# Kernel tuning notes

Hardware: AMD Instinct MI355X
Metric: run time of the kernel (lower is better)

Reference implementation:

```python
import jax, jax.numpy as jnp
import numpy as np

TEMPERATURE = 0.02


def setup_inputs() -> dict:
    key = jax.random.key(0)
    kq, kp = jax.random.split(key)
    query_embeddings = jax.random.normal(kq, (32, 32, 128), dtype=jnp.float32)      # [b, s, h]
    positive_embeddings = jax.random.normal(kp, (512, 128, 128), dtype=jnp.float32)  # [c, d, h]
    return {"query_embeddings": query_embeddings, "positive_embeddings": positive_embeddings}


def reference(query_embeddings, positive_embeddings):
    # Late interaction: all query tokens vs all doc tokens across the (in-)batch.
    # [b, c, s, d]
    late = jnp.einsum('bsh,cdh->bcsd', query_embeddings, positive_embeddings)
    # MaxSim: max over doc tokens, sum over query tokens -> [b, c]
    scores = late.max(axis=-1).sum(axis=-1) / TEMPERATURE
    # CrossEntropyLoss(reduction='mean') with labels = zeros(b)
    loss = jnp.mean(jax.nn.logsumexp(scores, axis=-1) - scores[:, 0])
    return loss
```

## Files before the change

kernel.cpp:

```cpp
#include <hip/hip_runtime.h>

#define BQ 32
#define H  128
#define C  512
#define D  128

typedef _Float16 half8v __attribute__((ext_vector_type(8)));
typedef float floatx4 __attribute__((ext_vector_type(4)));

__global__ __launch_bounds__(256) void qprep_kernel(const float* __restrict__ q,
                                                    _Float16* __restrict__ qs,
                                                    float* __restrict__ out) {
  int t = blockIdx.x * 256 + threadIdx.x;
  if (t == 0) out[0] = 0.0f;
  int lane = t & 63;
  int mt   = (t >> 6) & 1;
  int kb   = (t >> 7) & 3;
  int b    = t >> 9;
  int s    = mt * 16 + (lane & 15);
  int h    = kb * 32 + (lane >> 4) * 8;
  const float* src = q + ((b * 32 + s) * H + h);
  float4 v0 = *(const float4*)src;
  float4 v1 = *(const float4*)(src + 4);
  half8v o = { (_Float16)v0.x, (_Float16)v0.y, (_Float16)v0.z, (_Float16)v0.w,
               (_Float16)v1.x, (_Float16)v1.y, (_Float16)v1.z, (_Float16)v1.w };
  *(half8v*)(qs + (size_t)t * 8) = o;
}

__global__ __launch_bounds__(256, 2) void scores_kernel(const float* __restrict__ pos,
                                                        const _Float16* __restrict__ qs,
                                                        float* __restrict__ scores) {
  const int c    = blockIdx.x;
  const int tid  = threadIdx.x;
  const int w    = tid >> 6;
  const int lane = tid & 63;
  const int mt   = w & 1;
  const int half = w >> 1;
  const int ntg  = half * 4;
  const int quad = lane >> 4;
  const int nrow = lane & 15;

  __shared__ float pmm[BQ][2][32];

  const half8v* qf = (const half8v*)qs;
  const int abase  = mt * 64 + lane;
  const float* pc  = pos + (size_t)c * (D * H);

  half8v  bf[4][4];
  half8v  areg[2][4];
  floatx4 acc[2][4];

#pragma unroll
  for (int kb = 0; kb < 4; ++kb) areg[0][kb] = qf[abase + kb * 128];
#pragma unroll
  for (int kb = 0; kb < 4; ++kb) areg[1][kb] = qf[512 + abase + kb * 128];

#pragma unroll
  for (int kb = 0; kb < 4; ++kb)
#pragma unroll
    for (int nt = 0; nt < 4; ++nt) {
      const float* src = pc + ((ntg + nt) * 16 + nrow) * H + kb * 32 + quad * 8;
      float4 v0 = *(const float4*)src;
      float4 v1 = *(const float4*)(src + 4);
      half8v f = { (_Float16)v0.x, (_Float16)v0.y, (_Float16)v0.z, (_Float16)v0.w,
                   (_Float16)v1.x, (_Float16)v1.y, (_Float16)v1.z, (_Float16)v1.w };
      bf[kb][nt] = f;
    }

  auto reduce_store = [&](int b, floatx4* a) {
    float m0 = fmaxf(fmaxf(a[0][0], a[1][0]), fmaxf(a[2][0], a[3][0]));
    float m1 = fmaxf(fmaxf(a[0][1], a[1][1]), fmaxf(a[2][1], a[3][1]));
    float m2 = fmaxf(fmaxf(a[0][2], a[1][2]), fmaxf(a[2][2], a[3][2]));
    float m3 = fmaxf(fmaxf(a[0][3], a[1][3]), fmaxf(a[2][3], a[3][3]));
#pragma unroll
    for (int off = 1; off < 16; off <<= 1) {
      m0 = fmaxf(m0, __shfl_xor(m0, off));
      m1 = fmaxf(m1, __shfl_xor(m1, off));
      m2 = fmaxf(m2, __shfl_xor(m2, off));
      m3 = fmaxf(m3, __shfl_xor(m3, off));
    }
    if (nrow == 0) {
      float4 v = {m0, m1, m2, m3};
      *(float4*)&pmm[b][half][mt * 16 + quad * 4] = v;
    }
  };

#pragma unroll
  for (int nt = 0; nt < 4; ++nt) { floatx4 z = {0.f, 0.f, 0.f, 0.f}; acc[0][nt] = z; }
#pragma unroll
  for (int kb = 0; kb < 4; ++kb)
#pragma unroll
    for (int nt = 0; nt < 4; ++nt)
      acc[0][nt] = __builtin_amdgcn_mfma_f32_16x16x32_f16(areg[0][kb], bf[kb][nt], acc[0][nt], 0, 0, 0);

#pragma unroll
  for (int b = 1; b < BQ; ++b) {
    const int cur = b & 1, prv = cur ^ 1;
    if (b + 1 < BQ) {
      const int nb = (b + 1) * 512 + abase;
#pragma unroll
      for (int kb = 0; kb < 4; ++kb) areg[prv][kb] = qf[nb + kb * 128];
    }
#pragma unroll
    for (int nt = 0; nt < 4; ++nt) { floatx4 z = {0.f, 0.f, 0.f, 0.f}; acc[cur][nt] = z; }
#pragma unroll
    for (int kb = 0; kb < 4; ++kb)
#pragma unroll
      for (int nt = 0; nt < 4; ++nt)
        acc[cur][nt] = __builtin_amdgcn_mfma_f32_16x16x32_f16(areg[cur][kb], bf[kb][nt], acc[cur][nt], 0, 0, 0);
    reduce_store(b - 1, acc[prv]);
  }
  reduce_store(BQ - 1, acc[1]);

  __syncthreads();

  {
    int b  = tid >> 3;
    int sq = tid & 7;
    float4 x = *(float4*)&pmm[b][0][sq * 4];
    float4 y = *(float4*)&pmm[b][1][sq * 4];
    float v = fmaxf(x.x, y.x) + fmaxf(x.y, y.y) + fmaxf(x.z, y.z) + fmaxf(x.w, y.w);
    v += __shfl_xor(v, 1);
    v += __shfl_xor(v, 2);
    v += __shfl_xor(v, 4);
    if ((tid & 7) == 0) scores[b * C + c] = v * 50.0f;
  }
}

__global__ __launch_bounds__(256) void loss_kernel(const float* __restrict__ scores,
                                                   float* __restrict__ out) {
  __shared__ float red[8];
  const int b = blockIdx.x, tid = threadIdx.x, w = tid >> 6, lane = tid & 63;
  const float* row = scores + b * C;
  float x0 = row[tid], x1 = row[tid + 256];
  float mx = fmaxf(x0, x1);
#pragma unroll
  for (int off = 1; off < 64; off <<= 1) mx = fmaxf(mx, __shfl_xor(mx, off));
  if (lane == 0) red[w] = mx;
  __syncthreads();
  float bmax = fmaxf(fmaxf(red[0], red[1]), fmaxf(red[2], red[3]));
  float e = __expf(x0 - bmax) + __expf(x1 - bmax);
#pragma unroll
  for (int off = 1; off < 64; off <<= 1) e += __shfl_xor(e, off);
  if (lane == 0) red[4 + w] = e;
  __syncthreads();
  if (tid == 0) {
    float s = red[4] + red[5] + red[6] + red[7];
    atomicAdd(out, (bmax + __logf(s) - row[0]) * (1.0f / 32.0f));
  }
}

extern "C" void kernel_launch(void* const* d_in, const int* in_sizes, int n_in,
                              void* d_out, int out_size, void* d_ws, size_t ws_size,
                              hipStream_t stream) {
  const float* q = (const float*)d_in[0];
  const float* p = (const float*)d_in[1];
  float* scores  = (float*)d_ws;
  _Float16* qs   = (_Float16*)((char*)d_ws + 65536);

  qprep_kernel<<<64, 256, 0, stream>>>(q, qs, (float*)d_out);
  scores_kernel<<<C, 256, 0, stream>>>(p, qs, scores);
  loss_kernel<<<32, 256, 0, stream>>>(scores, (float*)d_out);
}
```

Measured before the change: 99.64 us.

## Swap MFMA operand roles so doc tokens are rows, cutting max-reduction shuffles

The doc tokens now go in the MFMA A operand (M dimension) and the query tokens in the B operand (N dimension). Each wave owns 32 doc rows and computes both 16-query tiles. The max over doc tokens can then be taken largely within each lane's accumulator registers, needing two cross-lane shuffles per value instead of four butterfly steps on four values. Each wave now loads all query fragments per batch, which doubles its query register loads and adds a four-way max across waves in shared memory.

```diff
diff --git a/kernel.cpp b/kernel.cpp
--- a/kernel.cpp
+++ b/kernel.cpp
@@ -14,10 +14,10 @@
   int t = blockIdx.x * 256 + threadIdx.x;
   if (t == 0) out[0] = 0.0f;
   int lane = t & 63;
-  int mt   = (t >> 6) & 1;
+  int st   = (t >> 6) & 1;
   int kb   = (t >> 7) & 3;
   int b    = t >> 9;
-  int s    = mt * 16 + (lane & 15);
+  int s    = st * 16 + (lane & 15);
   int h    = kb * 32 + (lane >> 4) * 8;
   const float* src = q + ((b * 32 + s) * H + h);
   float4 v0 = *(const float4*)src;
@@ -34,80 +34,86 @@
   const int tid  = threadIdx.x;
   const int w    = tid >> 6;
   const int lane = tid & 63;
-  const int mt   = w & 1;
-  const int half = w >> 1;
-  const int ntg  = half * 4;
   const int quad = lane >> 4;
-  const int nrow = lane & 15;
+  const int mrow = lane & 15;
 
-  __shared__ float pmm[BQ][2][32];
+  __shared__ float pmm[BQ][4][32];
 
   const half8v* qf = (const half8v*)qs;
-  const int abase  = mt * 64 + lane;
-  const float* pc  = pos + (size_t)c * (D * H);
+  const float*  pc = pos + (size_t)c * (D * H);
 
-  half8v  bf[4][4];
-  half8v  areg[2][4];
-  floatx4 acc[2][4];
+  half8v  pa[2][4];
+  half8v  qb[2][2][4];
+  floatx4 acc[2][2][2];
 
 #pragma unroll
-  for (int kb = 0; kb < 4; ++kb) areg[0][kb] = qf[abase + kb * 128];
+  for (int nt = 0; nt < 2; ++nt)
 #pragma unroll
-  for (int kb = 0; kb < 4; ++kb) areg[1][kb] = qf[512 + abase + kb * 128];
+    for (int kb = 0; kb < 4; ++kb) {
+      qb[0][nt][kb] = qf[(kb * 2 + nt) * 64 + lane];
+      qb[1][nt][kb] = qf[(( (1 * 4) + kb) * 2 + nt) * 64 + lane];
+    }
 
 #pragma unroll
   for (int kb = 0; kb < 4; ++kb)
 #pragma unroll
-    for (int nt = 0; nt < 4; ++nt) {
-      const float* src = pc + ((ntg + nt) * 16 + nrow) * H + kb * 32 + quad * 8;
+    for (int mt2 = 0; mt2 < 2; ++mt2) {
+      const float* src = pc + ((w * 32 + mt2 * 16 + mrow) * H + kb * 32 + quad * 8);
       float4 v0 = *(const float4*)src;
       float4 v1 = *(const float4*)(src + 4);
       half8v f = { (_Float16)v0.x, (_Float16)v0.y, (_Float16)v0.z, (_Float16)v0.w,
                    (_Float16)v1.x, (_Float16)v1.y, (_Float16)v1.z, (_Float16)v1.w };
-      bf[kb][nt] = f;
+      pa[mt2][kb] = f;
     }
 
-  auto reduce_store = [&](int b, floatx4* a) {
-    float m0 = fmaxf(fmaxf(a[0][0], a[1][0]), fmaxf(a[2][0], a[3][0]));
-    float m1 = fmaxf(fmaxf(a[0][1], a[1][1]), fmaxf(a[2][1], a[3][1]));
-    float m2 = fmaxf(fmaxf(a[0][2], a[1][2]), fmaxf(a[2][2], a[3][2]));
-    float m3 = fmaxf(fmaxf(a[0][3], a[1][3]), fmaxf(a[2][3], a[3][3]));
-#pragma unroll
-    for (int off = 1; off < 16; off <<= 1) {
-      m0 = fmaxf(m0, __shfl_xor(m0, off));
-      m1 = fmaxf(m1, __shfl_xor(m1, off));
-      m2 = fmaxf(m2, __shfl_xor(m2, off));
-      m3 = fmaxf(m3, __shfl_xor(m3, off));
-    }
-    if (nrow == 0) {
-      float4 v = {m0, m1, m2, m3};
-      *(float4*)&pmm[b][half][mt * 16 + quad * 4] = v;
-    }
+  auto reduce_store = [&](int b, floatx4 (&a)[2][2]) {
+    float t0 = fmaxf(fmaxf(fmaxf(a[0][0][0], a[0][0][1]), fmaxf(a[0][0][2], a[0][0][3])),
+                     fmaxf(fmaxf(a[1][0][0], a[1][0][1]), fmaxf(a[1][0][2], a[1][0][3])));
+    float t1 = fmaxf(fmaxf(fmaxf(a[0][1][0], a[0][1][1]), fmaxf(a[0][1][2], a[0][1][3])),
+                     fmaxf(fmaxf(a[1][1][0], a[1][1][1]), fmaxf(a[1][1][2], a[1][1][3])));
+    t0 = fmaxf(t0, __shfl_xor(t0, 16));
+    t0 = fmaxf(t0, __shfl_xor(t0, 32));
+    t1 = fmaxf(t1, __shfl_xor(t1, 16));
+    t1 = fmaxf(t1, __shfl_xor(t1, 32));
+    float v = (lane < 16) ? t0 : t1;
+    if (lane < 32) pmm[b][w][lane] = v;
   };
 
 #pragma unroll
-  for (int nt = 0; nt < 4; ++nt) { floatx4 z = {0.f, 0.f, 0.f, 0.f}; acc[0][nt] = z; }
+  for (int mt2 = 0; mt2 < 2; ++mt2)
+#pragma unroll
+    for (int nt = 0; nt < 2; ++nt) { floatx4 z = {0.f, 0.f, 0.f, 0.f}; acc[0][mt2][nt] = z; }
 #pragma unroll
   for (int kb = 0; kb < 4; ++kb)
 #pragma unroll
-    for (int nt = 0; nt < 4; ++nt)
-      acc[0][nt] = __builtin_amdgcn_mfma_f32_16x16x32_f16(areg[0][kb], bf[kb][nt], acc[0][nt], 0, 0, 0);
+    for (int mt2 = 0; mt2 < 2; ++mt2)
+#pragma unroll
+      for (int nt = 0; nt < 2; ++nt)
+        acc[0][mt2][nt] = __builtin_amdgcn_mfma_f32_16x16x32_f16(
+            pa[mt2][kb], qb[0][nt][kb], acc[0][mt2][nt], 0, 0, 0);
 
 #pragma unroll
   for (int b = 1; b < BQ; ++b) {
     const int cur = b & 1, prv = cur ^ 1;
     if (b + 1 < BQ) {
-      const int nb = (b + 1) * 512 + abase;
 #pragma unroll
-      for (int kb = 0; kb < 4; ++kb) areg[prv][kb] = qf[nb + kb * 128];
+      for (int nt = 0; nt < 2; ++nt)
+#pragma unroll
+        for (int kb = 0; kb < 4; ++kb)
+          qb[prv][nt][kb] = qf[(((b + 1) * 4 + kb) * 2 + nt) * 64 + lane];
     }
 #pragma unroll
-    for (int nt = 0; nt < 4; ++nt) { floatx4 z = {0.f, 0.f, 0.f, 0.f}; acc[cur][nt] = z; }
+    for (int mt2 = 0; mt2 < 2; ++mt2)
+#pragma unroll
+      for (int nt = 0; nt < 2; ++nt) { floatx4 z = {0.f, 0.f, 0.f, 0.f}; acc[cur][mt2][nt] = z; }
 #pragma unroll
     for (int kb = 0; kb < 4; ++kb)
 #pragma unroll
-      for (int nt = 0; nt < 4; ++nt)
-        acc[cur][nt] = __builtin_amdgcn_mfma_f32_16x16x32_f16(areg[cur][kb], bf[kb][nt], acc[cur][nt], 0, 0, 0);
+      for (int mt2 = 0; mt2 < 2; ++mt2)
+#pragma unroll
+        for (int nt = 0; nt < 2; ++nt)
+          acc[cur][mt2][nt] = __builtin_amdgcn_mfma_f32_16x16x32_f16(
+              pa[mt2][kb], qb[cur][nt][kb], acc[cur][mt2][nt], 0, 0, 0);
     reduce_store(b - 1, acc[prv]);
   }
   reduce_store(BQ - 1, acc[1]);
@@ -117,13 +123,19 @@
   {
     int b  = tid >> 3;
     int sq = tid & 7;
-    float4 x = *(float4*)&pmm[b][0][sq * 4];
-    float4 y = *(float4*)&pmm[b][1][sq * 4];
-    float v = fmaxf(x.x, y.x) + fmaxf(x.y, y.y) + fmaxf(x.z, y.z) + fmaxf(x.w, y.w);
+    float4 x0 = *(float4*)&pmm[b][0][sq * 4];
+    float4 x1 = *(float4*)&pmm[b][1][sq * 4];
+    float4 x2 = *(float4*)&pmm[b][2][sq * 4];
+    float4 x3 = *(float4*)&pmm[b][3][sq * 4];
+    float mx_x = fmaxf(fmaxf(x0.x, x1.x), fmaxf(x2.x, x3.x));
+    float mx_y = fmaxf(fmaxf(x0.y, x1.y), fmaxf(x2.y, x3.y));
+    float mx_z = fmaxf(fmaxf(x0.z, x1.z), fmaxf(x2.z, x3.z));
+    float mx_w = fmaxf(fmaxf(x0.w, x1.w), fmaxf(x2.w, x3.w));
+    float v = (mx_x + mx_y) + (mx_z + mx_w);
     v += __shfl_xor(v, 1);
     v += __shfl_xor(v, 2);
     v += __shfl_xor(v, 4);
-    if ((tid & 7) == 0) scores[b * C + c] = v * 50.0f;
+    if (sq == 0) scores[b * C + c] = v * 50.0f;
   }
 }
 
```

New measurement: 96.47 us. 1.03x faster.

## Swap MFMA operand roles so doc tokens occupy rows and max reduces in-register

Applied to the files above, without the earlier changes.

The MFMA operands are swapped: doc tokens become the A (row) operand and query tokens the B (column) operand. Each wave now owns 64 doc rows and 16 query tokens. The max over doc tokens can then be done mostly inside each lane's accumulator registers, with only two cross-lane shuffles instead of four shuffle rounds on four values. This adds a three-slot query prefetch ring and removes the separate accumulator zeroing. The cost is a different shared-memory layout and final combine, which may change register pressure.

```diff
diff --git a/kernel.cpp b/kernel.cpp
--- a/kernel.cpp
+++ b/kernel.cpp
@@ -14,10 +14,10 @@
   int t = blockIdx.x * 256 + threadIdx.x;
   if (t == 0) out[0] = 0.0f;
   int lane = t & 63;
-  int mt   = (t >> 6) & 1;
+  int sh   = (t >> 6) & 1;
   int kb   = (t >> 7) & 3;
   int b    = t >> 9;
-  int s    = mt * 16 + (lane & 15);
+  int s    = sh * 16 + (lane & 15);
   int h    = kb * 32 + (lane >> 4) * 8;
   const float* src = q + ((b * 32 + s) * H + h);
   float4 v0 = *(const float4*)src;
@@ -34,80 +34,75 @@
   const int tid  = threadIdx.x;
   const int w    = tid >> 6;
   const int lane = tid & 63;
-  const int mt   = w & 1;
-  const int half = w >> 1;
-  const int ntg  = half * 4;
+  const int dq   = w & 1;
+  const int sh   = w >> 1;
   const int quad = lane >> 4;
   const int nrow = lane & 15;
 
-  __shared__ float pmm[BQ][2][32];
+  __shared__ float pmm[BQ][4][16];
 
   const half8v* qf = (const half8v*)qs;
-  const int abase  = mt * 64 + lane;
-  const float* pc  = pos + (size_t)c * (D * H);
+  const float*  pc = pos + (size_t)c * (D * H);
 
-  half8v  bf[4][4];
-  half8v  areg[2][4];
+  half8v  pa[4][4];
+  half8v  qb[3][4];
   floatx4 acc[2][4];
-
-#pragma unroll
-  for (int kb = 0; kb < 4; ++kb) areg[0][kb] = qf[abase + kb * 128];
-#pragma unroll
-  for (int kb = 0; kb < 4; ++kb) areg[1][kb] = qf[512 + abase + kb * 128];
+  floatx4 zc = {0.f, 0.f, 0.f, 0.f};
 
 #pragma unroll
   for (int kb = 0; kb < 4; ++kb)
 #pragma unroll
-    for (int nt = 0; nt < 4; ++nt) {
-      const float* src = pc + ((ntg + nt) * 16 + nrow) * H + kb * 32 + quad * 8;
+    for (int mt = 0; mt < 4; ++mt) {
+      const float* src = pc + ((dq * 64 + mt * 16 + nrow) * H + kb * 32 + quad * 8);
       float4 v0 = *(const float4*)src;
       float4 v1 = *(const float4*)(src + 4);
       half8v f = { (_Float16)v0.x, (_Float16)v0.y, (_Float16)v0.z, (_Float16)v0.w,
                    (_Float16)v1.x, (_Float16)v1.y, (_Float16)v1.z, (_Float16)v1.w };
-      bf[kb][nt] = f;
+      pa[mt][kb] = f;
     }
 
-  auto reduce_store = [&](int b, floatx4* a) {
-    float m0 = fmaxf(fmaxf(a[0][0], a[1][0]), fmaxf(a[2][0], a[3][0]));
-    float m1 = fmaxf(fmaxf(a[0][1], a[1][1]), fmaxf(a[2][1], a[3][1]));
-    float m2 = fmaxf(fmaxf(a[0][2], a[1][2]), fmaxf(a[2][2], a[3][2]));
-    float m3 = fmaxf(fmaxf(a[0][3], a[1][3]), fmaxf(a[2][3], a[3][3]));
 #pragma unroll
-    for (int off = 1; off < 16; off <<= 1) {
-      m0 = fmaxf(m0, __shfl_xor(m0, off));
-      m1 = fmaxf(m1, __shfl_xor(m1, off));
-      m2 = fmaxf(m2, __shfl_xor(m2, off));
-      m3 = fmaxf(m3, __shfl_xor(m3, off));
-    }
-    if (nrow == 0) {
-      float4 v = {m0, m1, m2, m3};
-      *(float4*)&pmm[b][half][mt * 16 + quad * 4] = v;
-    }
+  for (int kb = 0; kb < 4; ++kb) qb[0][kb] = qf[(kb * 2 + sh) * 64 + lane];
+#pragma unroll
+  for (int kb = 0; kb < 4; ++kb) qb[1][kb] = qf[((4 + kb) * 2 + sh) * 64 + lane];
+
+  auto reduce_store = [&](int b, floatx4 (&a)[4]) {
+    float m0 = fmaxf(fmaxf(a[0][0], a[0][1]), fmaxf(a[0][2], a[0][3]));
+    float m1 = fmaxf(fmaxf(a[1][0], a[1][1]), fmaxf(a[1][2], a[1][3]));
+    float m2 = fmaxf(fmaxf(a[2][0], a[2][1]), fmaxf(a[2][2], a[2][3]));
+    float m3 = fmaxf(fmaxf(a[3][0], a[3][1]), fmaxf(a[3][2], a[3][3]));
+    float m  = fmaxf(fmaxf(m0, m1), fmaxf(m2, m3));
+    m = fmaxf(m, __shfl_xor(m, 16));
+    m = fmaxf(m, __shfl_xor(m, 32));
+    if (lane < 16) pmm[b][w][lane] = m;
   };
 
 #pragma unroll
-  for (int nt = 0; nt < 4; ++nt) { floatx4 z = {0.f, 0.f, 0.f, 0.f}; acc[0][nt] = z; }
+  for (int mt = 0; mt < 4; ++mt)
+    acc[0][mt] = __builtin_amdgcn_mfma_f32_16x16x32_f16(pa[mt][0], qb[0][0], zc, 0, 0, 0);
 #pragma unroll
-  for (int kb = 0; kb < 4; ++kb)
+  for (int kb = 1; kb < 4; ++kb)
 #pragma unroll
-    for (int nt = 0; nt < 4; ++nt)
-      acc[0][nt] = __builtin_amdgcn_mfma_f32_16x16x32_f16(areg[0][kb], bf[kb][nt], acc[0][nt], 0, 0, 0);
+    for (int mt = 0; mt < 4; ++mt)
+      acc[0][mt] = __builtin_amdgcn_mfma_f32_16x16x32_f16(pa[mt][kb], qb[0][kb], acc[0][mt], 0, 0, 0);
 
 #pragma unroll
   for (int b = 1; b < BQ; ++b) {
     const int cur = b & 1, prv = cur ^ 1;
     if (b + 1 < BQ) {
-      const int nb = (b + 1) * 512 + abase;
+      half8v* dst = qb[(b + 1) % 3];
 #pragma unroll
-      for (int kb = 0; kb < 4; ++kb) areg[prv][kb] = qf[nb + kb * 128];
+      for (int kb = 0; kb < 4; ++kb) dst[kb] = qf[(((b + 1) * 4 + kb) * 2 + sh) * 64 + lane];
     }
+    const half8v* qc = qb[b % 3];
 #pragma unroll
-    for (int nt = 0; nt < 4; ++nt) { floatx4 z = {0.f, 0.f, 0.f, 0.f}; acc[cur][nt] = z; }
+    for (int mt = 0; mt < 4; ++mt)
+      acc[cur][mt] = __builtin_amdgcn_mfma_f32_16x16x32_f16(pa[mt][0], qc[0], zc, 0, 0, 0);
 #pragma unroll
-    for (int kb = 0; kb < 4; ++kb)
+    for (int kb = 1; kb < 4; ++kb)
 #pragma unroll
-      for (int nt = 0; nt < 4; ++nt)
-        acc[cur][nt] = __builtin_amdgcn_mfma_f32_16x16x32_f16(areg[cur][kb], bf[kb][nt], acc[cur][nt], 0, 0, 0);
+      for (int mt = 0; mt < 4; ++mt)
+        acc[cur][mt] = __builtin_amdgcn_mfma_f32_16x16x32_f16(pa[mt][kb], qc[kb], acc[cur][mt], 0, 0, 0);
     reduce_store(b - 1, acc[prv]);
   }
   reduce_store(BQ - 1, acc[1]);
@@ -116,14 +111,18 @@
 
   {
     int b  = tid >> 3;
-    int sq = tid & 7;
-    float4 x = *(float4*)&pmm[b][0][sq * 4];
-    float4 y = *(float4*)&pmm[b][1][sq * 4];
-    float v = fmaxf(x.x, y.x) + fmaxf(x.y, y.y) + fmaxf(x.z, y.z) + fmaxf(x.w, y.w);
+    int t8 = tid & 7;
+    float v = 0.f;
+#pragma unroll
+    for (int j = 0; j < 4; ++j) {
+      int s  = t8 * 4 + j;
+      int h2 = s >> 4, sl = s & 15;
+      v += fmaxf(pmm[b][2 * h2][sl], pmm[b][2 * h2 + 1][sl]);
+    }
     v += __shfl_xor(v, 1);
     v += __shfl_xor(v, 2);
     v += __shfl_xor(v, 4);
-    if ((tid & 7) == 0) scores[b * C + c] = v * 50.0f;
+    if (t8 == 0) scores[b * C + c] = v * 50.0f;
   }
 }
 
```

Result: faster. 94.26 us (-5.4%).
